# Kernel tuning notes

Hardware: AMD Instinct MI355X
Metric: run time of the kernel (lower is better)

Reference implementation:

```python
import jax, jax.numpy as jnp
import numpy as np

B, N, D, K = 16, 1024, 512, 8
NUM_ITERS = 3
EPS = 1e-08
LN_EPS = 1e-05


def layer_norm(x, g, b):
    m = jnp.mean(x, axis=-1, keepdims=True)
    v = jnp.var(x, axis=-1, keepdims=True)
    return (x - m) * jax.lax.rsqrt(v + LN_EPS) * g + b


def setup_inputs() -> dict:
    key = jax.random.key(0)
    ks = jax.random.split(key, 8)
    s = 1.0 / np.sqrt(D)
    return {
        "embeddings": jax.random.normal(ks[0], (B, N, D), jnp.float32),
        "noise_init": jax.random.normal(ks[1], (B, K, D), jnp.float32),
        "noise_final": jax.random.normal(ks[2], (B, K, D), jnp.float32),
        "slots_mu": jax.random.normal(ks[3], (1, K, D), jnp.float32) * s,
        "slots_logsigma": jax.random.normal(ks[4], (1, K, D), jnp.float32) * s,
        "mixing_coeffs": jnp.ones((1, K), jnp.float32) / K,
        "Wk": jax.random.normal(ks[5], (D, D), jnp.float32) * s,
        "bk": jnp.zeros((D,), jnp.float32),
        "Wq": jax.random.normal(ks[6], (D, D), jnp.float32) * s,
        "bq": jnp.zeros((D,), jnp.float32),
        "Wv": jax.random.normal(ks[7], (D, D), jnp.float32) * s,
        "bv": jnp.zeros((D,), jnp.float32),
        "ln_g": jnp.ones((D,), jnp.float32),
        "ln_b": jnp.zeros((D,), jnp.float32),
    }


def reference(embeddings, noise_init, noise_final, slots_mu, slots_logsigma,
              mixing_coeffs, Wk, bk, Wq, bq, Wv, bv, ln_g, ln_b):
    b, n, d = embeddings.shape
    mixing = jnp.broadcast_to(mixing_coeffs, (b, K))           # [B,K]
    mu = jnp.broadcast_to(slots_mu, (b, K, d))                 # [B,K,D]
    sigma = jnp.exp(jnp.broadcast_to(slots_logsigma, (b, K, d)))
    slots = mu + sigma * noise_init                            # sampled slots

    x = layer_norm(embeddings, ln_g, ln_b)
    keys = x @ Wk + bk                                         # [B,N,D]
    values = x @ Wv + bv                                       # [B,N,D]
    # slots are never updated inside the loop, so queries are loop-invariant
    queries = slots @ Wq + bq                                  # [B,K,D]

    log2pi = jnp.float32(np.log(2.0 * np.pi))
    attn = None
    for _ in range(NUM_ITERS):
        diff = keys[:, :, None, :] - queries[:, None, :, :]    # [B,N,K,D]
        gll = -0.5 * jnp.sum(diff * diff / (sigma[:, None] ** 2 + EPS), axis=-1)  # [B,N,K]
        gll = (-0.5 * d * log2pi
               - 0.5 * jnp.sum(jnp.log(jnp.abs(sigma) + EPS), axis=-1)[:, None, :]
               + gll)
        attn = mixing[:, None, :] * gll                        # [B,N,K]
        attn = attn / jnp.sum(attn, axis=-1, keepdims=True)
        attn = attn / (jnp.sum(attn, axis=1, keepdims=True) + EPS)
        mu = jnp.einsum('bnk,bnd->bkd', attn, values)          # [B,K,D]
        diff2 = values[:, :, None, :] - mu[:, None, :, :]      # [B,N,K,D]
        sigma = jnp.einsum('bnk,bnkd->bkd', attn, diff2 * diff2)
        mixing = jnp.sum(attn, axis=1) / n

    sigma = jnp.maximum(jnp.abs(sigma), EPS)
    slots = mu + sigma * noise_final
    return slots, jnp.transpose(attn, (0, 2, 1))
```

## Files before the change

### kernel.cpp

```cpp
#include <hip/hip_runtime.h>
#include <math.h>

#define BB 16
#define NN 1024
#define DD 512
#define KK 8
#define EPS_ 1e-8f
#define LN_EPS_ 1e-5f
#define GLL_C0 (-470.4965290007924f)

typedef __attribute__((ext_vector_type(8))) short short8;
typedef __attribute__((ext_vector_type(4))) short short4v;
typedef __attribute__((ext_vector_type(4))) float f32x4;
typedef __attribute__((ext_vector_type(4))) int int4v;

static __device__ inline short f2bf(float f) {
    unsigned u = __builtin_bit_cast(unsigned, f);
    u = (u + 0x7fff + ((u >> 16) & 1)) >> 16;
    return (short)u;
}
static __device__ inline float bf2f(short s) {
    unsigned u = ((unsigned)(unsigned short)s) << 16;
    return __builtin_bit_cast(float, u);
}

struct Params {
    const float *emb, *noise_init, *noise_final, *slots_mu, *slots_logsg,
                *mixing_co, *Wk, *bk, *Wq, *bq, *Wv, *bv, *ln_g, *ln_b;
    float *out;
    float *queries, *attn;
    float *s1p, *s2p;
    float *off, *mix16, *colsum;
    float *ivtab;
    short *Abf, *Kbf, *Vbf, *WtKV, *WqT, *slotbf, *F_bt;
};

__global__ __launch_bounds__(256) void k_pre(Params p)
{
    __shared__ __align__(16) short eb[4352];
    int u = blockIdx.x, tid = threadIdx.x;
    if (u < 4096) {
        int row  = u * 4 + (tid >> 6);
        int lane = tid & 63;
        const float* e = p.emb + (size_t)row * DD + lane * 8;
        float4 v0 = *(const float4*)e;
        float4 v1 = *(const float4*)(e + 4);
        float v[8] = {v0.x, v0.y, v0.z, v0.w, v1.x, v1.y, v1.z, v1.w};
        float s = 0.0f;
#pragma unroll
        for (int j = 0; j < 8; j++) s += v[j];
#pragma unroll
        for (int off = 32; off; off >>= 1) s += __shfl_xor(s, off);
        float m = s * (1.0f / DD);
        float vs = 0.0f;
#pragma unroll
        for (int j = 0; j < 8; j++) { float d = v[j] - m; vs = fmaf(d, d, vs); }
#pragma unroll
        for (int off = 32; off; off >>= 1) vs += __shfl_xor(vs, off);
        float rstd = rsqrtf(vs * (1.0f / DD) + LN_EPS_);

        float4 g0 = *(const float4*)&p.ln_g[lane * 8];
        float4 g1 = *(const float4*)&p.ln_g[lane * 8 + 4];
        float4 b0 = *(const float4*)&p.ln_b[lane * 8];
        float4 b1 = *(const float4*)&p.ln_b[lane * 8 + 4];
        float g[8] = {g0.x, g0.y, g0.z, g0.w, g1.x, g1.y, g1.z, g1.w};
        float bb[8] = {b0.x, b0.y, b0.z, b0.w, b1.x, b1.y, b1.z, b1.w};
        short8 o;
#pragma unroll
        for (int j = 0; j < 8; j++) o[j] = f2bf(fmaf((v[j] - m) * rstd, g[j], bb[j]));
        *(short8*)&p.Abf[(size_t)row * DD + lane * 8] = o;
    } else if (u < 4864) {
        int idx = u - 4096;
        int z = idx >> 8, rem = idx & 255;
        const float* W = (z == 0) ? p.Wk : (z == 1) ? p.Wv : p.Wq;
        short* T; int nbase;
        if (z < 2) { T = p.WtKV; nbase = z * 512; } else { T = p.WqT; nbase = 0; }
        int k0 = (rem & 15) * 32, n0 = (rem >> 4) * 32;
        int tx = tid & 31, ty = tid >> 5;
        float (*t)[33] = (float (*)[33])eb;
#pragma unroll
        for (int q = 0; q < 4; q++)
            t[ty + q * 8][tx] = W[(size_t)(k0 + ty + q * 8) * DD + n0 + tx];
        __syncthreads();
#pragma unroll
        for (int q = 0; q < 4; q++)
            T[(size_t)(nbase + n0 + ty + q * 8) * DD + k0 + tx] = f2bf(t[tx][ty + q * 8]);
    } else {
        int idx = u - 4864;
        int b = idx >> 3, k = idx & 7;
        float* redf = (float*)eb;
        float ld = 0.0f;
#pragma unroll
        for (int q = 0; q < 2; q++) {
            int d = tid + q * 256;
            float sg = expf(p.slots_logsg[k * DD + d]);
            float sl = fmaf(sg, p.noise_init[((size_t)(b * KK + k)) * DD + d],
                            p.slots_mu[k * DD + d]);
            p.slotbf[((size_t)(b * KK + k)) * DD + d] = f2bf(sl);
            if (b == 0) p.ivtab[k * DD + d] = 1.0f / (sg * sg + EPS_);
            ld += logf(fabsf(sg) + EPS_);
        }
        {
            short4v zv = {0, 0, 0, 0};
            *(short4v*)&p.F_bt[(size_t)(b * 16 + 8 + k) * 1024 + tid * 4] = zv;
        }
        redf[tid] = ld;
        __syncthreads();
        for (int s = 128; s > 0; s >>= 1) {
            if (tid < s) redf[tid] += redf[tid + s];
            __syncthreads();
        }
        if (tid == 0) {
            p.off[b * 16 + k]       = GLL_C0 - 0.5f * redf[0];
            p.mix16[b * 16 + k]     = p.mixing_co[k];
            p.off[b * 16 + 8 + k]   = 0.0f;
            p.mix16[b * 16 + 8 + k] = 0.0f;
            p.colsum[b * KK + k]    = 0.0f;
        }
    }
}

__global__ __launch_bounds__(256) void k_gemm(Params p)
{
    __shared__ __align__(16) short smem[32768];
    int u = blockIdx.x, tid = threadIdx.x;
    int w = tid >> 6, l = tid & 63;
    int x, by, qmode;
    if (u >= 1024) { qmode = 1; x = u - 1024; if (x >= 4) return; by = 128; }
    else           { qmode = 0; x = u >> 7;   by = u & 127; }
    const short* A  = qmode ? p.slotbf : p.Abf + (size_t)by * 128 * DD;
    const short* Bt = qmode ? p.WqT : p.WtKV;
    int row0 = qmode ? 0 : by * 128;
    int col0 = x * 128;

    int sr = l >> 3;
    int sg_off = ((l & 7) ^ sr) * 8;
    int mq = (w & 1) * 64, nq = (w >> 1) * 64;
    int fr = l & 15;
    int orow = (l >> 4) * 4, ocol = l & 15;

    auto STAGE = [&](int k0, int buf) {
        short* As_ = smem + buf * 8192;
        short* Bs_ = smem + 16384 + buf * 8192;
#pragma unroll
        for (int j = 0; j < 4; j++) {
            int rbj = w * 32 + j * 8;
            int r   = rbj + sr;
            __builtin_amdgcn_global_load_lds(
                (const __attribute__((address_space(1))) unsigned int*)
                    (A + (size_t)r * DD + k0 + sg_off),
                (__attribute__((address_space(3))) unsigned int*)
                    &As_[rbj * 64 + l * 8], 16, 0, 0);
            __builtin_amdgcn_global_load_lds(
                (const __attribute__((address_space(1))) unsigned int*)
                    (Bt + (size_t)(col0 + r) * DD + k0 + sg_off),
                (__attribute__((address_space(3))) unsigned int*)
                    &Bs_[rbj * 64 + l * 8], 16, 0, 0);
        }
    };

    f32x4 acc[4][4] = {};
    STAGE(0, 0);
    __syncthreads();
    for (int i = 0; i < 8; i++) {
        if (i < 7) STAGE((i + 1) * 64, (i + 1) & 1);
        const short* As_ = smem + (i & 1) * 8192;
        const short* Bs_ = smem + 16384 + (i & 1) * 8192;
#pragma unroll
        for (int kk = 0; kk < 2; kk++) {
            int g = kk * 4 + (l >> 4);
            short8 af[4], bfv[4];
#pragma unroll
            for (int mi = 0; mi < 4; mi++)
                af[mi] = *(const short8*)&As_[(mq + mi * 16 + fr) * 64 + (g ^ (fr & 7)) * 8];
#pragma unroll
            for (int ni = 0; ni < 4; ni++)
                bfv[ni] = *(const short8*)&Bs_[(nq + ni * 16 + fr) * 64 + (g ^ (fr & 7)) * 8];
#pragma unroll
            for (int mi = 0; mi < 4; mi++)
#pragma unroll
                for (int ni = 0; ni < 4; ni++)
                    acc[mi][ni] = __builtin_amdgcn_mfma_f32_16x16x32_bf16(
                        af[mi], bfv[ni], acc[mi][ni], 0, 0, 0);
        }
        __syncthreads();
    }

    float bvv[4];
#pragma unroll
    for (int ni = 0; ni < 4; ni++) {
        int col = col0 + nq + ni * 16 + ocol;
        bvv[ni] = qmode ? p.bq[col] : (x < 4 ? p.bk[col] : p.bv[col - 512]);
    }

    if (qmode) {
        float* cpart = (float*)smem;
        if (tid < 128) cpart[tid] = 0.0f;
        __syncthreads();
#pragma unroll
        for (int ni = 0; ni < 4; ni++) {
            int col = col0 + nq + ni * 16 + ocol;
#pragma unroll
            for (int mi = 0; mi < 4; mi++)
#pragma unroll
                for (int r = 0; r < 4; r++) {
                    int row = mq + mi * 16 + orow + r;
                    float qv = acc[mi][ni][r] + bvv[ni];
                    p.queries[(size_t)row * DD + col] = qv;
                    float iv = p.ivtab[(row & 7) * DD + col];
                    int frow = (row >> 3) * 16 + (row & 7);
                    p.F_bt[(size_t)frow * 1024 + col]       = f2bf(-0.5f * iv);
                    p.F_bt[(size_t)frow * 1024 + 512 + col] = f2bf(qv * iv);
                    atomicAdd(&cpart[row], qv * qv * iv);
                }
        }
        __syncthreads();
        if (tid < 128)
            atomicAdd(&p.off[(tid >> 3) * 16 + (tid & 7)], -0.5f * cpart[tid]);
    } else {
        short* eb = smem;
        short* dst = (x < 4) ? p.Kbf : p.Vbf;
        int ccol0 = (x & 3) * 128;
#pragma unroll
        for (int mi = 0; mi < 4; mi++)
#pragma unroll
            for (int r = 0; r < 4; r++) {
                int row = mq + mi * 16 + orow + r;
                int sw = ((row >> 2) & 3) << 1;
#pragma unroll
                for (int ni = 0; ni < 4; ni++) {
                    int colg = nq + ni * 16 + ocol;
                    eb[row * 128 + (((colg >> 3) ^ sw) * 8) + (colg & 7)] =
                        f2bf(acc[mi][ni][r] + bvv[ni]);
                }
            }
        __syncthreads();
#pragma unroll
        for (int i = 0; i < 8; i++) {
            int row = i * 16 + w * 4 + (l >> 4);
            int c = l & 15;
            int cc = c ^ (((row >> 2) & 3) << 1);
            short8 vv = *(const short8*)&eb[row * 128 + cc * 8];
            *(short8*)&dst[(size_t)(row0 + row) * 512 + ccol0 + c * 8] = vv;
        }
    }
}

__global__ __launch_bounds__(512) void k_gllmu(Params p, int itlast)
{
    __shared__ f32x4 red[3][2][64];
    __shared__ float asml[64 * KK];
    int u = blockIdx.x, tid = threadIdx.x;
    int w = tid >> 6, l = tid & 63;
    int b = u >> 4, chunk = u & 15;
    int n0 = chunk * 64;
    int t = w & 1, ks = w >> 1;

    float csl = 0.0f;
#pragma unroll
    for (int st = 0; st < 2; st++) {
        const short* Ka = p.Kbf
            + ((size_t)(b * NN + n0 + st * 32 + t * 16 + (l & 15))) * 512
            + ks * 128 + (l >> 4) * 8;
        const short* Fi = p.F_bt + (size_t)(b * 16 + (l & 15)) * 1024
            + ks * 128 + (l >> 4) * 8;
        f32x4 acc0 = {}, acc1 = {};
#pragma unroll
        for (int j = 0; j < 4; j++) {
            short8 kf = *(const short8*)&Ka[j * 32];
            short8 f0 = *(const short8*)&Fi[j * 32];
            short8 f1 = *(const short8*)&Fi[j * 32 + 512];
            short8 k2;
#pragma unroll
            for (int e = 0; e < 8; e++) {
                float kv = bf2f(kf[e]);
                k2[e] = f2bf(kv * kv);
            }
            acc0 = __builtin_amdgcn_mfma_f32_16x16x32_bf16(k2, f0, acc0, 0, 0, 0);
            acc1 = __builtin_amdgcn_mfma_f32_16x16x32_bf16(kf, f1, acc1, 0, 0, 0);
        }
        f32x4 acc = acc0 + acc1;

        if (ks) red[ks - 1][t][l] = acc;
        __syncthreads();
        if (ks == 0) {
#pragma unroll
            for (int i = 0; i < 3; i++) acc += red[i][t][l];
            int col = l & 15;
            int rloc = st * 32 + t * 16 + (l >> 4) * 4;
            float offv = p.off[b * 16 + col];
            float mixv = p.mix16[b * 16 + col];
            float a[4], den[4];
#pragma unroll
            for (int r = 0; r < 4; r++) { a[r] = mixv * (acc[r] + offv); den[r] = a[r]; }
#pragma unroll
            for (int mask = 1; mask <= 8; mask <<= 1)
#pragma unroll
                for (int r = 0; r < 4; r++) den[r] += __shfl_xor(den[r], mask);
            if (col < KK) {
#pragma unroll
                for (int r = 0; r < 4; r++) {
                    float vv = a[r] / den[r];
                    asml[(rloc + r) * KK + col] = vv;
                    if (itlast)
                        p.attn[((size_t)(b * NN + n0 + rloc + r)) * KK + col] = vv;
                    csl += vv;
                }
            }
        }
        __syncthreads();
    }
    if (ks == 0) {
        csl += __shfl_xor(csl, 16);
        csl += __shfl_xor(csl, 32);
        if (l < KK) atomicAdd(&p.colsum[b * KK + l], csl);
    }

    float s1[KK] = {}, s2[KK] = {};
    const short* vb = p.Vbf + ((size_t)(b * NN + n0)) * DD + tid;
#pragma unroll 4
    for (int nn = 0; nn < 64; nn++) {
        float v = bf2f(vb[(size_t)nn * DD]);
        float vq = v * v;
        float4 a0 = *(const float4*)&asml[nn * KK];
        float4 a1 = *(const float4*)&asml[nn * KK + 4];
        float aa[8] = {a0.x, a0.y, a0.z, a0.w, a1.x, a1.y, a1.z, a1.w};
#pragma unroll
        for (int k = 0; k < KK; k++) {
            s1[k] = fmaf(aa[k], v, s1[k]);
            s2[k] = fmaf(aa[k], vq, s2[k]);
        }
    }
    size_t base = ((size_t)(b * 16 + chunk) * KK) * DD + tid;
#pragma unroll
    for (int k = 0; k < KK; k++) {
        p.s1p[base + (size_t)k * DD] = s1[k];
        p.s2p[base + (size_t)k * DD] = s2[k];
    }
}

__global__ __launch_bounds__(256) void k_fprep(Params p)
{
    __shared__ float red[512];
    int u = blockIdx.x, tid = threadIdx.x;
    int b = u >> 3, k = u & 7;
    float cs   = p.colsum[b * KK + k];
    float inv  = 1.0f / (cs + EPS_);
    float ssum = cs * inv;
    short* Fr = p.F_bt + (size_t)(b * 16 + k) * 1024;
    float* rc = red;
    float* rl = red + 256;
    float c = 0.0f, ld = 0.0f;
#pragma unroll
    for (int q = 0; q < 2; q++) {
        int d = tid * 2 + q;
        float s1 = 0.0f, s2 = 0.0f;
#pragma unroll
        for (int ns = 0; ns < 16; ns++) {
            size_t o = ((size_t)(b * 16 + ns) * KK + k) * DD + d;
            s1 += p.s1p[o];
            s2 += p.s2p[o];
        }
        float m  = s1 * inv;
        float sg = s2 * inv - m * m * (2.0f - ssum);
        float iv = 1.0f / (sg * sg + EPS_);
        float qv = p.queries[((size_t)(b * KK + k)) * DD + d];
        Fr[d]       = f2bf(-0.5f * iv);
        Fr[512 + d] = f2bf(qv * iv);
        c  = fmaf(qv * qv, iv, c);
        ld += logf(fabsf(sg) + EPS_);
    }
    rc[tid] = c; rl[tid] = ld;
    __syncthreads();
    for (int s = 128; s > 0; s >>= 1) {
        if (tid < s) { rc[tid] += rc[tid + s]; rl[tid] += rl[tid + s]; }
        __syncthreads();
    }
    if (tid == 0) {
        p.off[b * 16 + k]    = GLL_C0 - 0.5f * rl[0] - 0.5f * rc[0];
        p.mix16[b * 16 + k]  = ssum * (1.0f / NN);
        p.colsum[b * KK + k] = 0.0f;
    }
}

__global__ __launch_bounds__(256) void k_final(Params p)
{
    int u = blockIdx.x, tid = threadIdx.x;
    if (u < 256) {
        int gid = u * 256 + tid;
        int d = gid & 511;
        int k = (gid >> 9) & 7;
        int b = gid >> 12;
        float s1 = 0.0f, s2 = 0.0f;
#pragma unroll
        for (int ns = 0; ns < 16; ns++) {
            size_t o = ((size_t)(b * 16 + ns) * KK + k) * DD + d;
            s1 += p.s1p[o];
            s2 += p.s2p[o];
        }
        float cs   = p.colsum[b * KK + k];
        float inv  = 1.0f / (cs + EPS_);
        float ssum = cs * inv;
        float m    = s1 * inv;
        float sg   = s2 * inv - m * m * (2.0f - ssum);
        p.out[gid] = fmaf(fmaxf(fabsf(sg), EPS_), p.noise_final[gid], m);
    } else {
        int gid = (u - 256) * 256 + tid;
        int b = gid >> 13;
        int k = (gid >> 10) & 7;
        int n = gid & 1023;
        float cs = p.colsum[b * KK + k];
        p.out[BB * KK * DD + gid] =
            p.attn[((size_t)(b * NN + n)) * KK + k] / (cs + EPS_);
    }
}

extern "C" void kernel_launch(void* const* d_in, const int* in_sizes, int n_in,
                              void* d_out, int out_size, void* d_ws, size_t ws_size,
                              hipStream_t stream)
{
    Params pp;
    pp.emb         = (const float*)d_in[0];
    pp.noise_init  = (const float*)d_in[1];
    pp.noise_final = (const float*)d_in[2];
    pp.slots_mu    = (const float*)d_in[3];
    pp.slots_logsg = (const float*)d_in[4];
    pp.mixing_co   = (const float*)d_in[5];
    pp.Wk          = (const float*)d_in[6];
    pp.bk          = (const float*)d_in[7];
    pp.Wq          = (const float*)d_in[8];
    pp.bq          = (const float*)d_in[9];
    pp.Wv          = (const float*)d_in[10];
    pp.bv          = (const float*)d_in[11];
    pp.ln_g        = (const float*)d_in[12];
    pp.ln_b        = (const float*)d_in[13];
    pp.out         = (float*)d_out;

    float* ws = (float*)d_ws;
    pp.queries = ws;
    pp.attn    = pp.queries + BB * KK * DD;
    pp.s1p     = pp.attn + BB * NN * KK;
    pp.s2p     = pp.s1p + (size_t)BB * 16 * KK * DD;
    pp.off     = pp.s2p + (size_t)BB * 16 * KK * DD;
    pp.mix16   = pp.off + BB * 16;
    pp.colsum  = pp.mix16 + BB * 16;
    pp.ivtab   = pp.colsum + BB * KK;
    pp.Abf     = (short*)(pp.ivtab + KK * DD);
    pp.Kbf     = pp.Abf + (size_t)BB * NN * DD;
    pp.Vbf     = pp.Kbf + (size_t)BB * NN * DD;
    pp.WtKV    = pp.Vbf + (size_t)BB * NN * DD;
    pp.WqT     = pp.WtKV + (size_t)1024 * DD;
    pp.slotbf  = pp.WqT + (size_t)DD * DD;
    pp.F_bt    = pp.slotbf + (size_t)BB * KK * DD;

    k_pre<<<4992, 256, 0, stream>>>(pp);
    k_gemm<<<1032, 256, 0, stream>>>(pp);
    for (int it = 0; it < 3; it++) {
        k_gllmu<<<256, 512, 0, stream>>>(pp, it == 2);
        if (it < 2) k_fprep<<<128, 256, 0, stream>>>(pp);
    }
    k_final<<<768, 256, 0, stream>>>(pp);
}
```

Measured before the change: 222.5 us.

## Halve k_gllmu row chunk to double blocks and reduce qmode shared atomics

k_gllmu now processes 32 rows per block instead of 64 and launches 512 blocks, giving more parallelism across the 256 CUs. The number of partial-sum slices goes from 16 to 32, so k_fprep and k_final now read and reduce twice as many partials and the workspace layout changes to match. Separately, the qmode epilogue of the GEMM kernel now accumulates per-row sums in registers and reduces them with shuffles before one shared atomic per row group, which cuts shared-memory atomic traffic.

```diff
diff --git a/kernel.cpp b/kernel.cpp
--- a/kernel.cpp
+++ b/kernel.cpp
@@ -197,6 +197,11 @@
         float* cpart = (float*)smem;
         if (tid < 128) cpart[tid] = 0.0f;
         __syncthreads();
+        float csum[4][4];
+#pragma unroll
+        for (int mi = 0; mi < 4; mi++)
+#pragma unroll
+            for (int r = 0; r < 4; r++) csum[mi][r] = 0.0f;
 #pragma unroll
         for (int ni = 0; ni < 4; ni++) {
             int col = col0 + nq + ni * 16 + ocol;
@@ -211,7 +216,23 @@
                     int frow = (row >> 3) * 16 + (row & 7);
                     p.F_bt[(size_t)frow * 1024 + col]       = f2bf(-0.5f * iv);
                     p.F_bt[(size_t)frow * 1024 + 512 + col] = f2bf(qv * iv);
-                    atomicAdd(&cpart[row], qv * qv * iv);
+                    csum[mi][r] = fmaf(qv * qv, iv, csum[mi][r]);
+                }
+        }
+#pragma unroll
+        for (int mask = 1; mask <= 8; mask <<= 1)
+#pragma unroll
+            for (int mi = 0; mi < 4; mi++)
+#pragma unroll
+                for (int r = 0; r < 4; r++)
+                    csum[mi][r] += __shfl_xor(csum[mi][r], mask);
+        if ((l & 15) == 0) {
+#pragma unroll
+            for (int mi = 0; mi < 4; mi++)
+#pragma unroll
+                for (int r = 0; r < 4; r++) {
+                    int row = mq + mi * 16 + orow + r;
+                    atomicAdd(&cpart[row], csum[mi][r]);
                 }
         }
         __syncthreads();
@@ -249,77 +270,74 @@
 __global__ __launch_bounds__(512) void k_gllmu(Params p, int itlast)
 {
     __shared__ f32x4 red[3][2][64];
-    __shared__ float asml[64 * KK];
+    __shared__ float asml[32 * KK];
     int u = blockIdx.x, tid = threadIdx.x;
     int w = tid >> 6, l = tid & 63;
-    int b = u >> 4, chunk = u & 15;
-    int n0 = chunk * 64;
+    int b = u >> 5, chunk = u & 31;
+    int n0 = chunk * 32;
     int t = w & 1, ks = w >> 1;
 
-    float csl = 0.0f;
-#pragma unroll
-    for (int st = 0; st < 2; st++) {
-        const short* Ka = p.Kbf
-            + ((size_t)(b * NN + n0 + st * 32 + t * 16 + (l & 15))) * 512
-            + ks * 128 + (l >> 4) * 8;
-        const short* Fi = p.F_bt + (size_t)(b * 16 + (l & 15)) * 1024
-            + ks * 128 + (l >> 4) * 8;
-        f32x4 acc0 = {}, acc1 = {};
-#pragma unroll
-        for (int j = 0; j < 4; j++) {
-            short8 kf = *(const short8*)&Ka[j * 32];
-            short8 f0 = *(const short8*)&Fi[j * 32];
-            short8 f1 = *(const short8*)&Fi[j * 32 + 512];
-            short8 k2;
-#pragma unroll
-            for (int e = 0; e < 8; e++) {
-                float kv = bf2f(kf[e]);
-                k2[e] = f2bf(kv * kv);
+    const short* Ka = p.Kbf + ((size_t)(b * NN + n0 + t * 16 + (l & 15))) * 512
+                      + ks * 128 + (l >> 4) * 8;
+    const short* Fi = p.F_bt + (size_t)(b * 16 + (l & 15)) * 1024
+                      + ks * 128 + (l >> 4) * 8;
+    f32x4 acc0 = {}, acc1 = {};
+#pragma unroll
+    for (int j = 0; j < 4; j++) {
+        short8 kf = *(const short8*)&Ka[j * 32];
+        short8 f0 = *(const short8*)&Fi[j * 32];
+        short8 f1 = *(const short8*)&Fi[j * 32 + 512];
+        short8 k2;
+#pragma unroll
+        for (int e = 0; e < 8; e++) {
+            float kv = bf2f(kf[e]);
+            k2[e] = f2bf(kv * kv);
+        }
+        acc0 = __builtin_amdgcn_mfma_f32_16x16x32_bf16(k2, f0, acc0, 0, 0, 0);
+        acc1 = __builtin_amdgcn_mfma_f32_16x16x32_bf16(kf, f1, acc1, 0, 0, 0);
+    }
+    f32x4 acc = acc0 + acc1;
+
+    if (ks) red[ks - 1][t][l] = acc;
+    __syncthreads();
+    if (ks == 0) {
+#pragma unroll
+        for (int i = 0; i < 3; i++) acc += red[i][t][l];
+        int col = l & 15;
+        int rloc = t * 16 + (l >> 4) * 4;
+        float offv = p.off[b * 16 + col];
+        float mixv = p.mix16[b * 16 + col];
+        float a[4], den[4];
+#pragma unroll
+        for (int r = 0; r < 4; r++) {
+            a[r] = mixv * (acc[r] + offv);
+            den[r] = a[r];
+        }
+#pragma unroll
+        for (int mask = 1; mask <= 8; mask <<= 1)
+#pragma unroll
+            for (int r = 0; r < 4; r++) den[r] += __shfl_xor(den[r], mask);
+        float csl = 0.0f;
+        if (col < KK) {
+#pragma unroll
+            for (int r = 0; r < 4; r++) {
+                float vv = a[r] / den[r];
+                asml[(rloc + r) * KK + col] = vv;
+                if (itlast)
+                    p.attn[((size_t)(b * NN + n0 + rloc + r)) * KK + col] = vv;
+                csl += vv;
             }
-            acc0 = __builtin_amdgcn_mfma_f32_16x16x32_bf16(k2, f0, acc0, 0, 0, 0);
-            acc1 = __builtin_amdgcn_mfma_f32_16x16x32_bf16(kf, f1, acc1, 0, 0, 0);
-        }
-        f32x4 acc = acc0 + acc1;
-
-        if (ks) red[ks - 1][t][l] = acc;
-        __syncthreads();
-        if (ks == 0) {
-#pragma unroll
-            for (int i = 0; i < 3; i++) acc += red[i][t][l];
-            int col = l & 15;
-            int rloc = st * 32 + t * 16 + (l >> 4) * 4;
-            float offv = p.off[b * 16 + col];
-            float mixv = p.mix16[b * 16 + col];
-            float a[4], den[4];
-#pragma unroll
-            for (int r = 0; r < 4; r++) { a[r] = mixv * (acc[r] + offv); den[r] = a[r]; }
-#pragma unroll
-            for (int mask = 1; mask <= 8; mask <<= 1)
-#pragma unroll
-                for (int r = 0; r < 4; r++) den[r] += __shfl_xor(den[r], mask);
-            if (col < KK) {
-#pragma unroll
-                for (int r = 0; r < 4; r++) {
-                    float vv = a[r] / den[r];
-                    asml[(rloc + r) * KK + col] = vv;
-                    if (itlast)
-                        p.attn[((size_t)(b * NN + n0 + rloc + r)) * KK + col] = vv;
-                    csl += vv;
-                }
-            }
-        }
-        __syncthreads();
-    }
-    if (ks == 0) {
+        }
         csl += __shfl_xor(csl, 16);
         csl += __shfl_xor(csl, 32);
         if (l < KK) atomicAdd(&p.colsum[b * KK + l], csl);
     }
+    __syncthreads();
 
     float s1[KK] = {}, s2[KK] = {};
     const short* vb = p.Vbf + ((size_t)(b * NN + n0)) * DD + tid;
 #pragma unroll 4
-    for (int nn = 0; nn < 64; nn++) {
+    for (int nn = 0; nn < 32; nn++) {
         float v = bf2f(vb[(size_t)nn * DD]);
         float vq = v * v;
         float4 a0 = *(const float4*)&asml[nn * KK];
@@ -331,7 +349,7 @@
             s2[k] = fmaf(aa[k], vq, s2[k]);
         }
     }
-    size_t base = ((size_t)(b * 16 + chunk) * KK) * DD + tid;
+    size_t base = ((size_t)(b * 32 + chunk) * KK) * DD + tid;
 #pragma unroll
     for (int k = 0; k < KK; k++) {
         p.s1p[base + (size_t)k * DD] = s1[k];
@@ -356,8 +374,8 @@
         int d = tid * 2 + q;
         float s1 = 0.0f, s2 = 0.0f;
 #pragma unroll
-        for (int ns = 0; ns < 16; ns++) {
-            size_t o = ((size_t)(b * 16 + ns) * KK + k) * DD + d;
+        for (int ns = 0; ns < 32; ns++) {
+            size_t o = ((size_t)(b * 32 + ns) * KK + k) * DD + d;
             s1 += p.s1p[o];
             s2 += p.s2p[o];
         }
@@ -393,8 +411,8 @@
         int b = gid >> 12;
         float s1 = 0.0f, s2 = 0.0f;
 #pragma unroll
-        for (int ns = 0; ns < 16; ns++) {
-            size_t o = ((size_t)(b * 16 + ns) * KK + k) * DD + d;
+        for (int ns = 0; ns < 32; ns++) {
+            size_t o = ((size_t)(b * 32 + ns) * KK + k) * DD + d;
             s1 += p.s1p[o];
             s2 += p.s2p[o];
         }
@@ -440,8 +458,8 @@
     pp.queries = ws;
     pp.attn    = pp.queries + BB * KK * DD;
     pp.s1p     = pp.attn + BB * NN * KK;
-    pp.s2p     = pp.s1p + (size_t)BB * 16 * KK * DD;
-    pp.off     = pp.s2p + (size_t)BB * 16 * KK * DD;
+    pp.s2p     = pp.s1p + (size_t)BB * 32 * KK * DD;
+    pp.off     = pp.s2p + (size_t)BB * 32 * KK * DD;
     pp.mix16   = pp.off + BB * 16;
     pp.colsum  = pp.mix16 + BB * 16;
     pp.ivtab   = pp.colsum + BB * KK;
@@ -456,7 +474,7 @@
     k_pre<<<4992, 256, 0, stream>>>(pp);
     k_gemm<<<1032, 256, 0, stream>>>(pp);
     for (int it = 0; it < 3; it++) {
-        k_gllmu<<<256, 512, 0, stream>>>(pp, it == 2);
+        k_gllmu<<<512, 512, 0, stream>>>(pp, it == 2);
         if (it < 2) k_fprep<<<128, 256, 0, stream>>>(pp);
     }
     k_final<<<768, 256, 0, stream>>>(pp);
```

Result: faster. 201.4 us (-9.5%).
